# Optimization experiments

Measured on AMD Instinct MI355X. Metric: run time of the kernel, lower is better.

## Reference

```python
import jax, jax.numpy as jnp
import numpy as np

V, E, H, T, B = 32000, 256, 512, 64, 64
PAD = 0


def _gru(xg, h0, Whh, bhh, lens):
    """PyTorch-convention GRU. xg: [T,B,3H] precomputed input gates (W_ih x + b_ih).
    lens: [B] or None; if given, hidden state freezes at t >= lens[b] (packed-seq semantics)."""
    def step(h, inp):
        xg_t, t = inp
        hg = h @ Whh.T + bhh
        xr, xz, xn = jnp.split(xg_t, 3, axis=-1)
        hr, hz, hn = jnp.split(hg, 3, axis=-1)
        r = jax.nn.sigmoid(xr + hr)
        z = jax.nn.sigmoid(xz + hz)
        n = jnp.tanh(xn + r * hn)
        h_new = (1.0 - z) * n + z * h
        if lens is not None:
            h_new = jnp.where((t < lens)[:, None], h_new, h)
        return h_new, h_new
    steps = xg.shape[0]
    hT, outs = jax.lax.scan(step, h0, (xg, jnp.arange(steps)))
    return hT, outs


def setup_inputs() -> dict:
    key = jax.random.key(0)
    ks = jax.random.split(key, 13)
    s = 0.05
    return {
        "x": jax.random.randint(ks[0], (T, B), 0, V),
        "x_lens": jnp.maximum(jax.random.randint(ks[1], (B,), 0, T), 1),
        "y": jax.random.randint(ks[2], (T, B), 0, V),
        "emb": jax.random.normal(ks[3], (V, E), dtype=jnp.float32) * s,
        "enc_Wih": jax.random.normal(ks[4], (3 * H, E), dtype=jnp.float32) * s,
        "enc_Whh": jax.random.normal(ks[5], (3 * H, H), dtype=jnp.float32) * s,
        "enc_bih": jnp.zeros((3 * H,), jnp.float32),
        "enc_bhh": jnp.zeros((3 * H,), jnp.float32),
        "dec_Wih": jax.random.normal(ks[6], (3 * H, E), dtype=jnp.float32) * s,
        "dec_Whh": jax.random.normal(ks[7], (3 * H, H), dtype=jnp.float32) * s,
        "dec_bih": jnp.zeros((3 * H,), jnp.float32),
        "dec_bhh": jnp.zeros((3 * H,), jnp.float32),
        "Wout": jax.random.normal(ks[8], (V, H + E), dtype=jnp.float32) * s,
        "bout": jnp.zeros((V,), jnp.float32),
    }


def reference(x, x_lens, y, emb, enc_Wih, enc_Whh, enc_bih, enc_bhh,
              dec_Wih, dec_Whh, dec_bih, dec_bhh, Wout, bout):
    Tx, bs = x.shape
    # ---- encoder (dropout p=0 => identity) ----
    ex = emb[x]                                   # [T,B,E]
    xg = ex @ enc_Wih.T + enc_bih                 # [T,B,3H]
    h0 = jnp.zeros((bs, enc_Whh.shape[1]), emb.dtype)
    z, _ = _gru(xg, h0, enc_Whh, enc_bhh, x_lens)  # final hidden (packed semantics)
    # ---- decoder, fully teacher-forced (tf_ratio=1.0) ----
    ey = emb[y[:-1]]                              # [T-1,B,E]
    yg = ey @ dec_Wih.T + dec_bih
    _, dec_h = _gru(yg, z, dec_Whh, dec_bhh, None)  # [T-1,B,H]
    logits = jnp.concatenate([dec_h, ey], -1) @ Wout.T + bout  # [T-1,B,V]
    vocab = Wout.shape[0]
    dec_out = jnp.concatenate([jnp.zeros((1, bs, vocab), logits.dtype), logits], 0)
    # ---- CrossEntropy(ignore_index=PAD) over positions 1..T-1 ----
    tgt = y[1:].reshape(-1)
    lp = jax.nn.log_softmax(logits.reshape(-1, vocab), axis=-1)
    nll = -jnp.take_along_axis(lp, tgt[:, None], axis=1)[:, 0]
    mask = (tgt != PAD).astype(logits.dtype)
    loss = jnp.sum(nll * mask) / jnp.maximum(jnp.sum(mask), 1.0)
    return dec_out, loss
```

## Files before the change

kernel.cpp:

```cpp
#include <hip/hip_runtime.h>

typedef unsigned short u16;
typedef unsigned long long u64;
typedef __bf16 bf16x8 __attribute__((ext_vector_type(8)));
typedef float f32x4 __attribute__((ext_vector_type(4)));

#define AS1 __attribute__((address_space(1)))
#define AS3 __attribute__((address_space(3)))

__device__ __forceinline__ u16 f2bf(float f) {
  unsigned u = __builtin_bit_cast(unsigned, f);
  unsigned r = (u + 0x7FFFu + ((u >> 16) & 1u)) >> 16;
  return (u16)r;
}
__device__ __forceinline__ float bf2f(u16 h) {
  unsigned u = ((unsigned)h) << 16;
  return __builtin_bit_cast(float, u);
}

__device__ __forceinline__ u64 ld_coh_u64(const u64* p) {
  return __hip_atomic_load(p, __ATOMIC_RELAXED, __HIP_MEMORY_SCOPE_SYSTEM);
}
__device__ __forceinline__ void st_coh_u64(u64* p, u64 v) {
  __hip_atomic_store(p, v, __ATOMIC_RELAXED, __HIP_MEMORY_SCOPE_SYSTEM);
}

constexpr int V = 32000, E = 256, H = 512, T = 64, B = 64;
constexpr int H3 = 3 * H;
constexpr int MP = T * B;
constexpr int MD = (T - 1) * B;
constexpr int KO = H + E;
constexpr long long OUT_LOGITS_OFF = (long long)B * V;
constexpr long long OUT_LOSS_OFF  = (long long)T * B * V;

__global__ __launch_bounds__(256) void cast_weights(
    const float* __restrict__ eW, const float* __restrict__ dW,
    const float* __restrict__ oW,
    u16* __restrict__ eWb, u16* __restrict__ dWb, u16* __restrict__ oWb)
{
  size_t i = (size_t)blockIdx.x * 256 + threadIdx.x;
  const size_t S1 = (size_t)H3 * E;
  if (i < S1) { eWb[i] = f2bf(eW[i]); return; }
  i -= S1;
  if (i < S1) { dWb[i] = f2bf(dW[i]); return; }
  i -= S1;
  if (i < (size_t)V * KO) oWb[i] = f2bf(oW[i]);
}

__global__ __launch_bounds__(256) void gather_emb(
    const int* __restrict__ x, const int* __restrict__ y,
    const float* __restrict__ emb,
    u16* __restrict__ Aenc, u16* __restrict__ Afin)
{
  const int blk = blockIdx.x, e = threadIdx.x;
  if (blk < MP) {
    int tok = x[blk];
    Aenc[(size_t)blk * E + e] = f2bf(emb[(size_t)tok * E + e]);
  } else {
    int m = blk - MP;
    int tok = (m < MD) ? y[m] : 0;
    Afin[(size_t)m * KO + H + e] = f2bf(emb[(size_t)tok * E + e]);
  }
}

__global__ __launch_bounds__(256) void gemm_nt(
    const u16* __restrict__ A, int lda,
    const u16* __restrict__ W, int ldw,
    const float* __restrict__ bias,
    int Kt,
    float* __restrict__ Cf, u16* __restrict__ Cb,
    int ldc, int Mvalid)
{
  __shared__ u16 a_sm[128 * 32];
  __shared__ u16 b_sm[128 * 32];
  const int tid = threadIdx.x;
  const int lane = tid & 63;
  const int w = tid >> 6;
  const int m0 = blockIdx.x * 128;
  const int n0 = blockIdx.y * 128;
  const int srow = lane >> 2;
  const int gc = (lane & 3) ^ ((lane >> 3) & 3);
  const int r = lane & 15;
  const int q = lane >> 4;
  const int cx = (r >> 1) & 3;
  const int wr = w >> 1, wc = w & 1;

  f32x4 acc[4][4] = {};

  for (int kt = 0; kt < Kt; ++kt) {
    const int k0 = kt * 32;
    __syncthreads();
#pragma unroll
    for (int rr = 0; rr < 2; ++rr) {
      const int rbase = w * 32 + rr * 16;
      const u16* gA = A + (size_t)(m0 + rbase + srow) * lda + k0 + gc * 8;
      const u16* gB = W + (size_t)(n0 + rbase + srow) * ldw + k0 + gc * 8;
      __builtin_amdgcn_global_load_lds((const AS1 void*)gA,
                                       (AS3 void*)&a_sm[rbase * 32], 16, 0, 0);
      __builtin_amdgcn_global_load_lds((const AS1 void*)gB,
                                       (AS3 void*)&b_sm[rbase * 32], 16, 0, 0);
    }
    __syncthreads();
    bf16x8 af[4], bfv[4];
#pragma unroll
    for (int i = 0; i < 4; ++i) {
      af[i]  = *(const bf16x8*)&a_sm[(wr * 64 + i * 16 + r) * 32 + ((q ^ cx) * 8)];
      bfv[i] = *(const bf16x8*)&b_sm[(wc * 64 + i * 16 + r) * 32 + ((q ^ cx) * 8)];
    }
#pragma unroll
    for (int i = 0; i < 4; ++i)
#pragma unroll
      for (int j = 0; j < 4; ++j)
        acc[i][j] = __builtin_amdgcn_mfma_f32_16x16x32_bf16(af[i], bfv[j], acc[i][j], 0, 0, 0);
  }

#pragma unroll
  for (int i = 0; i < 4; ++i) {
#pragma unroll
    for (int j = 0; j < 4; ++j) {
      const int n = n0 + wc * 64 + j * 16 + r;
      const float bv = bias ? bias[n] : 0.f;
#pragma unroll
      for (int v = 0; v < 4; ++v) {
        const int m = m0 + wr * 64 + i * 16 + q * 4 + v;
        if (m < Mvalid) {
          const float val = acc[i][j][v] + bv;
          if (Cf) Cf[(size_t)m * ldc + n] = val;
          else    Cb[(size_t)m * ldc + n] = f2bf(val);
        }
      }
    }
  }
}

__global__ __launch_bounds__(512, 2) void gemm_big(
    const u16* __restrict__ A,
    const u16* __restrict__ W,
    const float* __restrict__ bias,
    float* __restrict__ C)
{
  extern __shared__ u16 sm[];
  const int tid = threadIdx.x;
  const int lane = tid & 63, w = tid >> 6;
  const int wr = w >> 2, wc = w & 3;
  const int r = lane & 15, q = lane >> 4;

  const int bid = blockIdx.x;
  const int swz = (bid & 7) * 250 + (bid >> 3);
  const int mt = swz & 15, nt = swz >> 4;
  const int m0 = mt * 256, n0 = nt * 256;

  const int rowq = tid >> 2;
  const int gl = (tid & 3) ^ ((tid >> 3) & 3);
  const u16* gA0 = A + (size_t)(m0 + rowq) * KO + gl * 8;
  const u16* gA1 = A + (size_t)(m0 + 128 + rowq) * KO + gl * 8;
  const u16* gW0 = W + (size_t)(n0 + rowq) * KO + gl * 8;
  const u16* gW1 = W + (size_t)(n0 + 128 + rowq) * KO + gl * 8;

  auto stage = [&](int c, int kt) {
    u16* ab = sm + c * 16384;
    u16* bb = ab + 8192;
    const int k0 = kt * 32;
    __builtin_amdgcn_global_load_lds((const AS1 void*)(gA0 + k0),
                                     (AS3 void*)(ab + w * 512), 16, 0, 0);
    __builtin_amdgcn_global_load_lds((const AS1 void*)(gW0 + k0),
                                     (AS3 void*)(bb + w * 512), 16, 0, 0);
    __builtin_amdgcn_global_load_lds((const AS1 void*)(gA1 + k0),
                                     (AS3 void*)(ab + 4096 + w * 512), 16, 0, 0);
    __builtin_amdgcn_global_load_lds((const AS1 void*)(gW1 + k0),
                                     (AS3 void*)(bb + 4096 + w * 512), 16, 0, 0);
  };

  const int qa = q ^ ((r >> 1) & 3);
  int aoff[8], boff[4];
#pragma unroll
  for (int i = 0; i < 8; ++i) aoff[i] = (wr * 128 + i * 16 + r) * 32 + qa * 8;
#pragma unroll
  for (int j = 0; j < 4; ++j) boff[j] = (wc * 64 + j * 16 + r) * 32 + qa * 8;

  f32x4 acc[8][4] = {};

  stage(0, 0);
  stage(1, 1);
  stage(2, 2);

  for (int kt = 0; kt < 24; ++kt) {
    const int c = kt % 3;
    if (kt < 22)      asm volatile("s_waitcnt vmcnt(8)" ::: "memory");
    else if (kt < 23) asm volatile("s_waitcnt vmcnt(4)" ::: "memory");
    else              asm volatile("s_waitcnt vmcnt(0)" ::: "memory");
    __builtin_amdgcn_s_barrier();
    __builtin_amdgcn_sched_barrier(0);

    const u16* ab = sm + c * 16384;
    const u16* bb = ab + 8192;
    bf16x8 fa[8], fb[4];
#pragma unroll
    for (int i = 0; i < 8; ++i) fa[i] = *(const bf16x8*)&ab[aoff[i]];
#pragma unroll
    for (int j = 0; j < 4; ++j) fb[j] = *(const bf16x8*)&bb[boff[j]];
    asm volatile("s_waitcnt lgkmcnt(0)" ::: "memory");
    __builtin_amdgcn_sched_barrier(0);
    __builtin_amdgcn_s_barrier();
    __builtin_amdgcn_sched_barrier(0);

    if (kt + 3 < 24) stage(c, kt + 3);

    __builtin_amdgcn_s_setprio(1);
#pragma unroll
    for (int i = 0; i < 8; ++i)
#pragma unroll
      for (int j = 0; j < 4; ++j)
        acc[i][j] = __builtin_amdgcn_mfma_f32_16x16x32_bf16(fa[i], fb[j], acc[i][j], 0, 0, 0);
    __builtin_amdgcn_s_setprio(0);
  }

#pragma unroll
  for (int j = 0; j < 4; ++j) {
    const int n = n0 + wc * 64 + j * 16 + r;
    const float bv = bias[n];
#pragma unroll
    for (int i = 0; i < 8; ++i) {
      const int mbase = m0 + wr * 128 + i * 16 + q * 4;
#pragma unroll
      for (int v = 0; v < 4; ++v) {
        const int m = mbase + v;
        if (m < MD)
          __builtin_nontemporal_store(acc[i][j][v] + bv, &C[(size_t)m * V + n]);
      }
    }
  }
}

__global__ __launch_bounds__(256) void gru_kernel(
    const u16* __restrict__ xgates,
    const float* __restrict__ Whh,
    const float* __restrict__ bhh,
    const int* __restrict__ lens,
    const float* __restrict__ h0,
    float* __restrict__ hf0, float* __restrict__ hf1,
    u16* __restrict__ hb0, u16* __restrict__ hb1,
    int steps, unsigned* __restrict__ bar,
    u16* __restrict__ outA)
{
  extern __shared__ char smem[];
  u16* whh_sm = (u16*)smem;
  u16* h_sm   = (u16*)(smem + 48 * 520 * 2);
  float* hg_sm = (float*)(smem + 112 * 520 * 2);

  const int tid = threadIdx.x;
  const int lane = tid & 63;
  const int w = tid >> 6;
  const int jbase = blockIdx.x * 16;
  const int r = lane & 15, q = lane >> 4;

  for (int e = tid; e < 48 * 512; e += 256) {
    int rowl = e >> 9, k = e & 511;
    int g = rowl >> 4, jl = rowl & 15;
    whh_sm[rowl * 520 + k] = f2bf(Whh[(size_t)(g * 512 + jbase + jl) * 512 + k]);
  }

  const int eb  = tid >> 2;
  const int jl0 = (tid & 3) * 4;
  const int jg0 = jbase + jl0;

  {
    u16 hb4[4];
#pragma unroll
    for (int v2 = 0; v2 < 4; ++v2) {
      float v = h0 ? h0[eb * 512 + jg0 + v2] : 0.f;
      hf0[eb * 512 + jg0 + v2] = v;
      hb4[v2] = f2bf(v);
    }
    u64 pack = (u64)hb4[0] | ((u64)hb4[1] << 16) | ((u64)hb4[2] << 32) |
               ((u64)hb4[3] << 48);
    st_coh_u64((u64*)&hb0[eb * 512 + jg0], pack);
  }
  asm volatile("s_waitcnt vmcnt(0)" ::: "memory");
  __syncthreads();
  if (tid == 0) {
    __hip_atomic_fetch_add(bar, 1u, __ATOMIC_RELAXED, __HIP_MEMORY_SCOPE_SYSTEM);
    while (__hip_atomic_load(bar, __ATOMIC_RELAXED, __HIP_MEMORY_SCOPE_SYSTEM) < 32u)
      __builtin_amdgcn_s_sleep(1);
  }
  __syncthreads();

  for (int t = 0; t < steps; ++t) {
    const float* hf_cur = (t & 1) ? hf1 : hf0;
    const u16*   hb_cur = (t & 1) ? hb1 : hb0;
    float*       hf_nxt = (t & 1) ? hf0 : hf1;
    u16*         hb_nxt = (t & 1) ? hb0 : hb1;

    const size_t mrow = (size_t)t * 64 + eb;
    u64 xrv = *(const u64*)&xgates[mrow * 1536 + jg0];
    u64 xzv = *(const u64*)&xgates[mrow * 1536 + 512 + jg0];
    u64 xnv = *(const u64*)&xgates[mrow * 1536 + 1024 + jg0];

    {
      const u64* src = (const u64*)hb_cur;
      u64 v[32];
#pragma unroll
      for (int i = 0; i < 32; ++i) v[i] = ld_coh_u64(src + i * 256 + tid);
#pragma unroll
      for (int i = 0; i < 32; ++i) {
        int c = i * 256 + tid;
        int row = c >> 7, c4 = c & 127;
        *(u64*)&h_sm[row * 520 + c4 * 4] = v[i];
      }
    }
    __syncthreads();

    f32x4 acc[3] = {};
#pragma unroll
    for (int kt = 0; kt < 16; ++kt) {
      bf16x8 a = *(const bf16x8*)&h_sm[(w * 16 + r) * 520 + kt * 32 + q * 8];
#pragma unroll
      for (int g = 0; g < 3; ++g) {
        bf16x8 bb = *(const bf16x8*)&whh_sm[(g * 16 + r) * 520 + kt * 32 + q * 8];
        acc[g] = __builtin_amdgcn_mfma_f32_16x16x32_bf16(a, bb, acc[g], 0, 0, 0);
      }
    }
#pragma unroll
    for (int g = 0; g < 3; ++g)
#pragma unroll
      for (int v = 0; v < 4; ++v)
        hg_sm[((w * 16 + q * 4 + v) * 3 + g) * 16 + r] = acc[g][v];
    __syncthreads();

    {
      u16 hb4[4];
#pragma unroll
      for (int v2 = 0; v2 < 4; ++v2) {
        const int jl = jl0 + v2, jg = jg0 + v2;
        float xr = bf2f((u16)(xrv >> (16 * v2)));
        float xz = bf2f((u16)(xzv >> (16 * v2)));
        float xn = bf2f((u16)(xnv >> (16 * v2)));
        float hr = hg_sm[(eb * 3 + 0) * 16 + jl] + bhh[jg];
        float hz = hg_sm[(eb * 3 + 1) * 16 + jl] + bhh[512 + jg];
        float hn = hg_sm[(eb * 3 + 2) * 16 + jl] + bhh[1024 + jg];
        float rg = 1.f / (1.f + __expf(-(xr + hr)));
        float zg = 1.f / (1.f + __expf(-(xz + hz)));
        float ng = tanhf(xn + rg * hn);
        float hold = hf_cur[eb * 512 + jg];
        float hnew = (1.f - zg) * ng + zg * hold;
        if (lens && t >= lens[eb]) hnew = hold;
        hf_nxt[eb * 512 + jg] = hnew;
        hb4[v2] = f2bf(hnew);
        if (outA) outA[mrow * (size_t)KO + jg] = hb4[v2];
      }
      u64 pack = (u64)hb4[0] | ((u64)hb4[1] << 16) | ((u64)hb4[2] << 32) |
                 ((u64)hb4[3] << 48);
      st_coh_u64((u64*)&hb_nxt[eb * 512 + jg0], pack);
    }

    asm volatile("s_waitcnt vmcnt(0)" ::: "memory");
    __syncthreads();
    if (tid == 0) {
      __hip_atomic_fetch_add(bar, 1u, __ATOMIC_RELAXED, __HIP_MEMORY_SCOPE_SYSTEM);
      const unsigned tgt = 32u * (unsigned)(t + 2);
      while (__hip_atomic_load(bar, __ATOMIC_RELAXED, __HIP_MEMORY_SCOPE_SYSTEM) < tgt)
        __builtin_amdgcn_s_sleep(1);
    }
    __syncthreads();
  }
}

__global__ __launch_bounds__(256) void loss_rows(
    const float* __restrict__ logits, const int* __restrict__ y,
    float* __restrict__ accum)
{
  __shared__ float sm_m[256], sm_s[256];
  const int row = blockIdx.x;
  const float* rp = logits + (size_t)row * V;
  const int tid = threadIdx.x;
  float m = -1e30f, s = 0.f;
  for (int it = 0; it < 32; ++it) {
    int i4 = tid + it * 256;
    if (i4 < V / 4) {
      float4 x = ((const float4*)rp)[i4];
      float mx = fmaxf(fmaxf(x.x, x.y), fmaxf(x.z, x.w));
      float mn = fmaxf(m, mx);
      s = s * __expf(m - mn) + __expf(x.x - mn) + __expf(x.y - mn) +
          __expf(x.z - mn) + __expf(x.w - mn);
      m = mn;
    }
  }
  sm_m[tid] = m; sm_s[tid] = s;
  __syncthreads();
  for (int off = 128; off > 0; off >>= 1) {
    if (tid < off) {
      float m2 = sm_m[tid + off], s2 = sm_s[tid + off];
      float mn = fmaxf(sm_m[tid], m2);
      sm_s[tid] = sm_s[tid] * __expf(sm_m[tid] - mn) + s2 * __expf(m2 - mn);
      sm_m[tid] = mn;
    }
    __syncthreads();
  }
  if (tid == 0) {
    int tgt = y[row + 64];
    float lse = sm_m[0] + __logf(sm_s[0]);
    float nll = lse - rp[tgt];
    if (tgt != 0) {
      atomicAdd(&accum[0], nll);
      atomicAdd(&accum[1], 1.f);
    }
  }
}

__global__ void finalize_loss(const float* __restrict__ accum, float* __restrict__ out) {
  out[0] = accum[0] / fmaxf(accum[1], 1.f);
}

extern "C" void kernel_launch(void* const* d_in, const int* in_sizes, int n_in,
                              void* d_out, int out_size, void* d_ws, size_t ws_size,
                              hipStream_t stream)
{
  const int*   x      = (const int*)d_in[0];
  const int*   x_lens = (const int*)d_in[1];
  const int*   y      = (const int*)d_in[2];
  const float* emb    = (const float*)d_in[3];
  const float* eWih   = (const float*)d_in[4];
  const float* eWhh   = (const float*)d_in[5];
  const float* ebih   = (const float*)d_in[6];
  const float* ebhh   = (const float*)d_in[7];
  const float* dWih   = (const float*)d_in[8];
  const float* dWhh   = (const float*)d_in[9];
  const float* dbih   = (const float*)d_in[10];
  const float* dbhh   = (const float*)d_in[11];
  const float* Wout   = (const float*)d_in[12];
  const float* bout   = (const float*)d_in[13];
  float* out = (float*)d_out;

  char* ws = (char*)d_ws;
  unsigned* cnt  = (unsigned*)(ws + 0);
  float*    accum = (float*)(ws + 8);
  u16*   Aenc = (u16*)(ws + 256);
  u16*   Afin = (u16*)(ws + 2097408);
  u16*   xg   = (u16*)(ws + 8388864);
  u16*   yg   = (u16*)(ws + 20971776);
  u16*   WEb  = (u16*)(ws + 33554688);
  u16*   WDb  = (u16*)(ws + 34341120);
  u16*   WOb  = (u16*)(ws + 35127552);
  float* hEf  = (float*)(ws + 84279552);
  u16*   hEb  = (u16*)(ws + 84541696);
  float* hDf  = (float*)(ws + 84672768);
  u16*   hDb  = (u16*)(ws + 84934912);

  hipMemsetAsync(d_out, 0, (size_t)B * V * sizeof(float), stream);
  hipMemsetAsync(ws, 0, 256, stream);

  cast_weights<<<99072, 256, 0, stream>>>(eWih, dWih, Wout, WEb, WDb, WOb);
  gather_emb<<<2 * MP, 256, 0, stream>>>(x, y, emb, Aenc, Afin);

  gemm_nt<<<dim3(32, 12), 256, 0, stream>>>(Aenc, E, WEb, E, ebih, E / 32,
                                            nullptr, xg, H3, MP);
  gemm_nt<<<dim3(32, 12), 256, 0, stream>>>(Afin + H, KO, WDb, E, dbih, E / 32,
                                            nullptr, yg, H3, MP);

  const size_t gru_lds = (size_t)112 * 520 * 2 + (size_t)64 * 3 * 16 * 4;
  gru_kernel<<<32, 256, gru_lds, stream>>>(xg, eWhh, ebhh, x_lens, nullptr,
      hEf, hEf + 32768, hEb, hEb + 32768, T, cnt + 0, nullptr);
  gru_kernel<<<32, 256, gru_lds, stream>>>(yg, dWhh, dbhh, nullptr, hEf,
      hDf, hDf + 32768, hDb, hDb + 32768, T - 1, cnt + 1, Afin);

  gemm_big<<<2000, 512, 3 * 16384 * sizeof(u16), stream>>>(
      Afin, WOb, bout, out + OUT_LOGITS_OFF);

  loss_rows<<<MD, 256, 0, stream>>>(out + OUT_LOGITS_OFF, y, accum);
  finalize_loss<<<1, 1, 0, stream>>>(accum, out + OUT_LOSS_OFF);
}
```

Baseline: 1.843 ms.

## Fuse decoder GRU with output projection GEMM via progress-counter overlap

```diff
diff --git a/kernel.cpp b/kernel.cpp
--- a/kernel.cpp
+++ b/kernel.cpp
@@ -133,106 +133,8 @@
   }
 }
 
-__global__ __launch_bounds__(512, 2) void gemm_big(
-    const u16* __restrict__ A,
-    const u16* __restrict__ W,
-    const float* __restrict__ bias,
-    float* __restrict__ C)
-{
-  extern __shared__ u16 sm[];
-  const int tid = threadIdx.x;
-  const int lane = tid & 63, w = tid >> 6;
-  const int wr = w >> 2, wc = w & 3;
-  const int r = lane & 15, q = lane >> 4;
-
-  const int bid = blockIdx.x;
-  const int swz = (bid & 7) * 250 + (bid >> 3);
-  const int mt = swz & 15, nt = swz >> 4;
-  const int m0 = mt * 256, n0 = nt * 256;
-
-  const int rowq = tid >> 2;
-  const int gl = (tid & 3) ^ ((tid >> 3) & 3);
-  const u16* gA0 = A + (size_t)(m0 + rowq) * KO + gl * 8;
-  const u16* gA1 = A + (size_t)(m0 + 128 + rowq) * KO + gl * 8;
-  const u16* gW0 = W + (size_t)(n0 + rowq) * KO + gl * 8;
-  const u16* gW1 = W + (size_t)(n0 + 128 + rowq) * KO + gl * 8;
-
-  auto stage = [&](int c, int kt) {
-    u16* ab = sm + c * 16384;
-    u16* bb = ab + 8192;
-    const int k0 = kt * 32;
-    __builtin_amdgcn_global_load_lds((const AS1 void*)(gA0 + k0),
-                                     (AS3 void*)(ab + w * 512), 16, 0, 0);
-    __builtin_amdgcn_global_load_lds((const AS1 void*)(gW0 + k0),
-                                     (AS3 void*)(bb + w * 512), 16, 0, 0);
-    __builtin_amdgcn_global_load_lds((const AS1 void*)(gA1 + k0),
-                                     (AS3 void*)(ab + 4096 + w * 512), 16, 0, 0);
-    __builtin_amdgcn_global_load_lds((const AS1 void*)(gW1 + k0),
-                                     (AS3 void*)(bb + 4096 + w * 512), 16, 0, 0);
-  };
-
-  const int qa = q ^ ((r >> 1) & 3);
-  int aoff[8], boff[4];
-#pragma unroll
-  for (int i = 0; i < 8; ++i) aoff[i] = (wr * 128 + i * 16 + r) * 32 + qa * 8;
-#pragma unroll
-  for (int j = 0; j < 4; ++j) boff[j] = (wc * 64 + j * 16 + r) * 32 + qa * 8;
-
-  f32x4 acc[8][4] = {};
-
-  stage(0, 0);
-  stage(1, 1);
-  stage(2, 2);
-
-  for (int kt = 0; kt < 24; ++kt) {
-    const int c = kt % 3;
-    if (kt < 22)      asm volatile("s_waitcnt vmcnt(8)" ::: "memory");
-    else if (kt < 23) asm volatile("s_waitcnt vmcnt(4)" ::: "memory");
-    else              asm volatile("s_waitcnt vmcnt(0)" ::: "memory");
-    __builtin_amdgcn_s_barrier();
-    __builtin_amdgcn_sched_barrier(0);
-
-    const u16* ab = sm + c * 16384;
-    const u16* bb = ab + 8192;
-    bf16x8 fa[8], fb[4];
-#pragma unroll
-    for (int i = 0; i < 8; ++i) fa[i] = *(const bf16x8*)&ab[aoff[i]];
-#pragma unroll
-    for (int j = 0; j < 4; ++j) fb[j] = *(const bf16x8*)&bb[boff[j]];
-    asm volatile("s_waitcnt lgkmcnt(0)" ::: "memory");
-    __builtin_amdgcn_sched_barrier(0);
-    __builtin_amdgcn_s_barrier();
-    __builtin_amdgcn_sched_barrier(0);
-
-    if (kt + 3 < 24) stage(c, kt + 3);
-
-    __builtin_amdgcn_s_setprio(1);
-#pragma unroll
-    for (int i = 0; i < 8; ++i)
-#pragma unroll
-      for (int j = 0; j < 4; ++j)
-        acc[i][j] = __builtin_amdgcn_mfma_f32_16x16x32_bf16(fa[i], fb[j], acc[i][j], 0, 0, 0);
-    __builtin_amdgcn_s_setprio(0);
-  }
-
-#pragma unroll
-  for (int j = 0; j < 4; ++j) {
-    const int n = n0 + wc * 64 + j * 16 + r;
-    const float bv = bias[n];
-#pragma unroll
-    for (int i = 0; i < 8; ++i) {
-      const int mbase = m0 + wr * 128 + i * 16 + q * 4;
-#pragma unroll
-      for (int v = 0; v < 4; ++v) {
-        const int m = mbase + v;
-        if (m < MD)
-          __builtin_nontemporal_store(acc[i][j][v] + bv, &C[(size_t)m * V + n]);
-      }
-    }
-  }
-}
-
-__global__ __launch_bounds__(256) void gru_kernel(
+template<int NT>
+__device__ __forceinline__ void gru_body(
     const u16* __restrict__ xgates,
     const float* __restrict__ Whh,
     const float* __restrict__ bhh,
@@ -241,9 +143,9 @@
     float* __restrict__ hf0, float* __restrict__ hf1,
     u16* __restrict__ hb0, u16* __restrict__ hb1,
     int steps, unsigned* __restrict__ bar,
-    u16* __restrict__ outA)
-{
-  extern __shared__ char smem[];
+    u16* __restrict__ outA,
+    int blk, char* smem)
+{
   u16* whh_sm = (u16*)smem;
   u16* h_sm   = (u16*)(smem + 48 * 520 * 2);
   float* hg_sm = (float*)(smem + 112 * 520 * 2);
@@ -251,20 +153,20 @@
   const int tid = threadIdx.x;
   const int lane = tid & 63;
   const int w = tid >> 6;
-  const int jbase = blockIdx.x * 16;
+  const int jbase = blk * 16;
   const int r = lane & 15, q = lane >> 4;
 
-  for (int e = tid; e < 48 * 512; e += 256) {
+  for (int e = tid; e < 48 * 512; e += NT) {
     int rowl = e >> 9, k = e & 511;
     int g = rowl >> 4, jl = rowl & 15;
     whh_sm[rowl * 520 + k] = f2bf(Whh[(size_t)(g * 512 + jbase + jl) * 512 + k]);
   }
 
-  const int eb  = tid >> 2;
+  const int eb  = (tid & 255) >> 2;
   const int jl0 = (tid & 3) * 4;
   const int jg0 = jbase + jl0;
 
-  {
+  if (tid < 256) {
     u16 hb4[4];
 #pragma unroll
     for (int v2 = 0; v2 < 4; ++v2) {
@@ -291,43 +193,49 @@
     float*       hf_nxt = (t & 1) ? hf0 : hf1;
     u16*         hb_nxt = (t & 1) ? hb0 : hb1;
 
+    u64 xrv = 0, xzv = 0, xnv = 0;
     const size_t mrow = (size_t)t * 64 + eb;
-    u64 xrv = *(const u64*)&xgates[mrow * 1536 + jg0];
-    u64 xzv = *(const u64*)&xgates[mrow * 1536 + 512 + jg0];
-    u64 xnv = *(const u64*)&xgates[mrow * 1536 + 1024 + jg0];
+    if (tid < 256) {
+      xrv = *(const u64*)&xgates[mrow * 1536 + jg0];
+      xzv = *(const u64*)&xgates[mrow * 1536 + 512 + jg0];
+      xnv = *(const u64*)&xgates[mrow * 1536 + 1024 + jg0];
+    }
 
     {
+      constexpr int NCH = 8192 / NT;
       const u64* src = (const u64*)hb_cur;
-      u64 v[32];
-#pragma unroll
-      for (int i = 0; i < 32; ++i) v[i] = ld_coh_u64(src + i * 256 + tid);
-#pragma unroll
-      for (int i = 0; i < 32; ++i) {
-        int c = i * 256 + tid;
+      u64 v[NCH];
+#pragma unroll
+      for (int i = 0; i < NCH; ++i) v[i] = ld_coh_u64(src + i * NT + tid);
+#pragma unroll
+      for (int i = 0; i < NCH; ++i) {
+        int c = i * NT + tid;
         int row = c >> 7, c4 = c & 127;
         *(u64*)&h_sm[row * 520 + c4 * 4] = v[i];
       }
     }
     __syncthreads();
 
-    f32x4 acc[3] = {};
-#pragma unroll
-    for (int kt = 0; kt < 16; ++kt) {
-      bf16x8 a = *(const bf16x8*)&h_sm[(w * 16 + r) * 520 + kt * 32 + q * 8];
-#pragma unroll
-      for (int g = 0; g < 3; ++g) {
-        bf16x8 bb = *(const bf16x8*)&whh_sm[(g * 16 + r) * 520 + kt * 32 + q * 8];
-        acc[g] = __builtin_amdgcn_mfma_f32_16x16x32_bf16(a, bb, acc[g], 0, 0, 0);
+    if (w < 4) {
+      f32x4 acc[3] = {};
+#pragma unroll
+      for (int kt = 0; kt < 16; ++kt) {
+        bf16x8 a = *(const bf16x8*)&h_sm[(w * 16 + r) * 520 + kt * 32 + q * 8];
+#pragma unroll
+        for (int g = 0; g < 3; ++g) {
+          bf16x8 bb = *(const bf16x8*)&whh_sm[(g * 16 + r) * 520 + kt * 32 + q * 8];
+          acc[g] = __builtin_amdgcn_mfma_f32_16x16x32_bf16(a, bb, acc[g], 0, 0, 0);
+        }
       }
-    }
-#pragma unroll
-    for (int g = 0; g < 3; ++g)
-#pragma unroll
-      for (int v = 0; v < 4; ++v)
-        hg_sm[((w * 16 + q * 4 + v) * 3 + g) * 16 + r] = acc[g][v];
-    __syncthreads();
-
-    {
+#pragma unroll
+      for (int g = 0; g < 3; ++g)
+#pragma unroll
+        for (int v = 0; v < 4; ++v)
+          hg_sm[((w * 16 + q * 4 + v) * 3 + g) * 16 + r] = acc[g][v];
+    }
+    __syncthreads();
+
+    if (tid < 256) {
       u16 hb4[4];
 #pragma unroll
       for (int v2 = 0; v2 < 4; ++v2) {
@@ -346,10 +254,10 @@
         if (lens && t >= lens[eb]) hnew = hold;
         hf_nxt[eb * 512 + jg] = hnew;
         hb4[v2] = f2bf(hnew);
-        if (outA) outA[mrow * (size_t)KO + jg] = hb4[v2];
       }
       u64 pack = (u64)hb4[0] | ((u64)hb4[1] << 16) | ((u64)hb4[2] << 32) |
                  ((u64)hb4[3] << 48);
+      if (outA) st_coh_u64((u64*)&outA[mrow * (size_t)KO + jg0], pack);
       st_coh_u64((u64*)&hb_nxt[eb * 512 + jg0], pack);
     }
 
@@ -362,6 +270,140 @@
         __builtin_amdgcn_s_sleep(1);
     }
     __syncthreads();
+  }
+}
+
+__global__ __launch_bounds__(256) void gru_kernel(
+    const u16* __restrict__ xgates, const float* __restrict__ Whh,
+    const float* __restrict__ bhh, const int* __restrict__ lens,
+    const float* __restrict__ h0,
+    float* __restrict__ hf0, float* __restrict__ hf1,
+    u16* __restrict__ hb0, u16* __restrict__ hb1,
+    int steps, unsigned* __restrict__ bar, u16* __restrict__ outA)
+{
+  extern __shared__ char smem[];
+  gru_body<256>(xgates, Whh, bhh, lens, h0, hf0, hf1, hb0, hb1, steps, bar,
+                outA, blockIdx.x, smem);
+}
+
+__global__ __launch_bounds__(512, 2) void fused_dec(
+    const u16* __restrict__ yg, const float* __restrict__ Whh,
+    const float* __restrict__ bhh, const float* __restrict__ h0,
+    float* __restrict__ hf0, float* __restrict__ hf1,
+    u16* __restrict__ hb0, u16* __restrict__ hb1,
+    unsigned* __restrict__ bar,
+    u16* __restrict__ afin,
+    const u16* __restrict__ W,
+    const float* __restrict__ bias,
+    float* __restrict__ C)
+{
+  extern __shared__ char smem[];
+
+  if (blockIdx.x < 32) {
+    gru_body<512>(yg, Whh, bhh, nullptr, h0, hf0, hf1, hb0, hb1, T - 1, bar,
+                  afin, blockIdx.x, smem);
+    return;
+  }
+
+  u16* sm = (u16*)smem;
+  const int wid = blockIdx.x - 32;
+  const int tid = threadIdx.x;
+  const int lane = tid & 63, w = tid >> 6;
+  const int wr = w >> 2, wc = w & 3;
+  const int r = lane & 15, q = lane >> 4;
+  const int rowq = tid >> 2;
+  const int gl = (tid & 3) ^ ((tid >> 3) & 3);
+  const int qa = q ^ ((r >> 1) & 3);
+
+  int aoff[8], boff[4];
+#pragma unroll
+  for (int i = 0; i < 8; ++i) aoff[i] = (wr * 128 + i * 16 + r) * 32 + qa * 8;
+#pragma unroll
+  for (int j = 0; j < 4; ++j) boff[j] = (wc * 64 + j * 16 + r) * 32 + qa * 8;
+
+  for (int tile = wid; tile < 2000; tile += 224) {
+    const int mt = tile / 125, nt = tile - mt * 125;
+    const int m0 = mt * 256, n0 = nt * 256;
+
+    int need = 4 * mt + 3; if (need > 62) need = 62;
+    const unsigned tgt = 32u * (unsigned)(need + 2);
+    if (tid == 0) {
+      while (__hip_atomic_load(bar, __ATOMIC_RELAXED, __HIP_MEMORY_SCOPE_SYSTEM) < tgt)
+        __builtin_amdgcn_s_sleep(16);
+    }
+    __syncthreads();
+
+    const u16* gA0 = afin + (size_t)(m0 + rowq) * KO + gl * 8;
+    const u16* gA1 = afin + (size_t)(m0 + 128 + rowq) * KO + gl * 8;
+    const u16* gW0 = W + (size_t)(n0 + rowq) * KO + gl * 8;
+    const u16* gW1 = W + (size_t)(n0 + 128 + rowq) * KO + gl * 8;
+
+    auto stage = [&](int c, int kt) {
+      u16* ab = sm + c * 16384;
+      u16* bb = ab + 8192;
+      const int k0 = kt * 32;
+      __builtin_amdgcn_global_load_lds((const AS1 void*)(gA0 + k0),
+                                       (AS3 void*)(ab + w * 512), 16, 0, 0);
+      __builtin_amdgcn_global_load_lds((const AS1 void*)(gW0 + k0),
+                                       (AS3 void*)(bb + w * 512), 16, 0, 0);
+      __builtin_amdgcn_global_load_lds((const AS1 void*)(gA1 + k0),
+                                       (AS3 void*)(ab + 4096 + w * 512), 16, 0, 0);
+      __builtin_amdgcn_global_load_lds((const AS1 void*)(gW1 + k0),
+                                       (AS3 void*)(bb + 4096 + w * 512), 16, 0, 0);
+    };
+
+    f32x4 acc[8][4] = {};
+
+    stage(0, 0);
+    stage(1, 1);
+    stage(2, 2);
+
+    for (int kt = 0; kt < 24; ++kt) {
+      const int c = kt % 3;
+      if (kt < 22)      asm volatile("s_waitcnt vmcnt(8)" ::: "memory");
+      else if (kt < 23) asm volatile("s_waitcnt vmcnt(4)" ::: "memory");
+      else              asm volatile("s_waitcnt vmcnt(0)" ::: "memory");
+      __builtin_amdgcn_s_barrier();
+      __builtin_amdgcn_sched_barrier(0);
+
+      const u16* ab = sm + c * 16384;
+      const u16* bb = ab + 8192;
+      bf16x8 fa[8], fb[4];
+#pragma unroll
+      for (int i = 0; i < 8; ++i) fa[i] = *(const bf16x8*)&ab[aoff[i]];
+#pragma unroll
+      for (int j = 0; j < 4; ++j) fb[j] = *(const bf16x8*)&bb[boff[j]];
+      asm volatile("s_waitcnt lgkmcnt(0)" ::: "memory");
+      __builtin_amdgcn_sched_barrier(0);
+      __builtin_amdgcn_s_barrier();
+      __builtin_amdgcn_sched_barrier(0);
+
+      if (kt + 3 < 24) stage(c, kt + 3);
+
+      __builtin_amdgcn_s_setprio(1);
+#pragma unroll
+      for (int i = 0; i < 8; ++i)
+#pragma unroll
+        for (int j = 0; j < 4; ++j)
+          acc[i][j] = __builtin_amdgcn_mfma_f32_16x16x32_bf16(fa[i], fb[j], acc[i][j], 0, 0, 0);
+      __builtin_amdgcn_s_setprio(0);
+    }
+
+#pragma unroll
+    for (int j = 0; j < 4; ++j) {
+      const int n = n0 + wc * 64 + j * 16 + r;
+      const float bv = bias[n];
+#pragma unroll
+      for (int i = 0; i < 8; ++i) {
+        const int mbase = m0 + wr * 128 + i * 16 + q * 4;
+#pragma unroll
+        for (int v = 0; v < 4; ++v) {
+          const int m = mbase + v;
+          if (m < MD)
+            __builtin_nontemporal_store(acc[i][j][v] + bv, &C[(size_t)m * V + n]);
+        }
+      }
+    }
   }
 }
 
@@ -460,11 +502,10 @@
   const size_t gru_lds = (size_t)112 * 520 * 2 + (size_t)64 * 3 * 16 * 4;
   gru_kernel<<<32, 256, gru_lds, stream>>>(xg, eWhh, ebhh, x_lens, nullptr,
       hEf, hEf + 32768, hEb, hEb + 32768, T, cnt + 0, nullptr);
-  gru_kernel<<<32, 256, gru_lds, stream>>>(yg, dWhh, dbhh, nullptr, hEf,
-      hDf, hDf + 32768, hDb, hDb + 32768, T - 1, cnt + 1, Afin);
-
-  gemm_big<<<2000, 512, 3 * 16384 * sizeof(u16), stream>>>(
-      Afin, WOb, bout, out + OUT_LOGITS_OFF);
+
+  fused_dec<<<256, 512, gru_lds, stream>>>(yg, dWhh, dbhh, hEf,
+      hDf, hDf + 32768, hDb, hDb + 32768, cnt + 1, Afin,
+      WOb, bout, out + OUT_LOGITS_OFF);
 
   loss_rows<<<MD, 256, 0, stream>>>(out + OUT_LOGITS_OFF, y, accum);
   finalize_loss<<<1, 1, 0, stream>>>(accum, out + OUT_LOSS_OFF);
```

Measured after the change: 1.785 ms. 1.03x faster.
